# Kernel optimization log

Hardware: AMD Instinct MI355X
Metric: run time of the kernel (lower is better)

## Reference

```python
import jax, jax.numpy as jnp
import numpy as np


def setup_inputs() -> dict:
    key = jax.random.key(0)
    k1, k2, k3 = jax.random.split(key, 3)
    B, H, F, O = 2048, 512, 128, 10
    inputs = jax.random.normal(k1, (B, F), dtype=jnp.float32)
    # centers ~ uniform(-1, 1) as in init_params
    centers = jax.random.uniform(k2, (H, F), dtype=jnp.float32, minval=-1.0, maxval=1.0)
    sigma = jnp.ones((1,), dtype=jnp.float32)
    W = jax.random.normal(k3, (O, H), dtype=jnp.float32) * (1.0 / np.sqrt(H))
    b = jnp.zeros((O,), dtype=jnp.float32)
    return {"inputs": inputs, "centers": centers, "sigma": sigma, "W": W, "b": b}


def reference(inputs, centers, sigma, W, b):
    # pairwise squared distances: [B, H, F] diff -> sum over F -> [B, H]
    diff = inputs[:, None, :] - centers[None, :, :]
    distances = jnp.sum(diff * diff, axis=-1)  # [B, H]
    rbf = jnp.exp(-distances / (2.0 * sigma[0] ** 2))  # [B, H]
    # linear: y = rbf @ W.T + b
    return rbf @ W.T + b
```

## Files before the change

### kernel.cpp

```cpp
#include <hip/hip_runtime.h>


constexpr int Fdim = 128;
constexpr int Hdim = 512;
constexpr int Odim = 10;
constexpr int BM   = 8;
constexpr int KC   = 32;
constexpr int NCH  = Fdim / KC;
constexpr int LDC  = 513;
constexpr int LDXT = 12;
constexpr int LDR  = 516;

__global__ __launch_bounds__(512, 1) void rbf_all(
    const float* __restrict__ x,
    const float* __restrict__ c,
    const float* __restrict__ sigmap,
    const float* __restrict__ W,
    const float* __restrict__ bias,
    float* __restrict__ out)
{
    __shared__ float cT[KC][LDC];
    __shared__ float xT[Fdim][LDXT];
    __shared__ float W_s[Odim][Hdim];
    __shared__ float rbf_s[BM][LDR];
    __shared__ float xn_s[BM];
    __shared__ float cn_s[Hdim];

    const int tid  = threadIdx.x;
    const int lane = tid & 63;
    const int wave = tid >> 6;
    const int wr   = wave >> 2;
    const int wh   = wave & 3;
    const int row0 = blockIdx.x * BM;

    const float4* x4 = reinterpret_cast<const float4*>(x);
    const float4* c4 = reinterpret_cast<const float4*>(c);

#pragma unroll
    for (int k = 0; k < (Odim * Hdim) / 512; ++k) {
        int idx = tid + 512 * k;
        W_s[idx >> 9][idx & 511] = W[idx];
    }

    if (tid < 256) {
        int r  = tid >> 5;
        int fq = tid & 31;
        float4 v = x4[(size_t)(row0 + r) * (Fdim / 4) + fq];
        xT[4 * fq + 0][r] = v.x;
        xT[4 * fq + 1][r] = v.y;
        xT[4 * fq + 2][r] = v.z;
        xT[4 * fq + 3][r] = v.w;
        float s = v.x * v.x + v.y * v.y + v.z * v.z + v.w * v.w;
#pragma unroll
        for (int sft = 1; sft < 32; sft <<= 1) s += __shfl_xor(s, sft, 64);
        if (fq == 0) xn_s[r] = s;
    }

    const int f4 = tid & 7;
    const int hh = tid >> 3;

    float4 pre[8];
    float cn_part[8];
#pragma unroll
    for (int p = 0; p < 8; ++p) cn_part[p] = 0.0f;

#pragma unroll
    for (int p = 0; p < 8; ++p)
        pre[p] = c4[(size_t)(hh + 64 * p) * (Fdim / 4) + f4];
#pragma unroll
    for (int p = 0; p < 8; ++p) {
        float4 v = pre[p];
        int h = hh + 64 * p;
        cT[4 * f4 + 0][h] = v.x;
        cT[4 * f4 + 1][h] = v.y;
        cT[4 * f4 + 2][h] = v.z;
        cT[4 * f4 + 3][h] = v.w;
        cn_part[p] += v.x * v.x + v.y * v.y + v.z * v.z + v.w * v.w;
    }
    __syncthreads();

    float acc[4][2];
#pragma unroll
    for (int i = 0; i < 4; ++i) { acc[i][0] = 0.0f; acc[i][1] = 0.0f; }

    for (int k = 0; k < NCH; ++k) {
        if (k + 1 < NCH) {
#pragma unroll
            for (int p = 0; p < 8; ++p)
                pre[p] = c4[(size_t)(hh + 64 * p) * (Fdim / 4) + (k + 1) * (KC / 4) + f4];
        }

#pragma unroll 8
        for (int f = 0; f < KC; ++f) {
            float4 xv = *reinterpret_cast<const float4*>(&xT[k * KC + f][4 * wr]);
            float2 cv = *reinterpret_cast<const float2*>(&cT[f][wh * 128 + 2 * lane]);
            acc[0][0] = fmaf(xv.x, cv.x, acc[0][0]);
            acc[0][1] = fmaf(xv.x, cv.y, acc[0][1]);
            acc[1][0] = fmaf(xv.y, cv.x, acc[1][0]);
            acc[1][1] = fmaf(xv.y, cv.y, acc[1][1]);
            acc[2][0] = fmaf(xv.z, cv.x, acc[2][0]);
            acc[2][1] = fmaf(xv.z, cv.y, acc[2][1]);
            acc[3][0] = fmaf(xv.w, cv.x, acc[3][0]);
            acc[3][1] = fmaf(xv.w, cv.y, acc[3][1]);
        }

        if (k + 1 < NCH) {
            __syncthreads();
#pragma unroll
            for (int p = 0; p < 8; ++p) {
                float4 v = pre[p];
                int h = hh + 64 * p;
                cT[4 * f4 + 0][h] = v.x;
                cT[4 * f4 + 1][h] = v.y;
                cT[4 * f4 + 2][h] = v.z;
                cT[4 * f4 + 3][h] = v.w;
                cn_part[p] += v.x * v.x + v.y * v.y + v.z * v.z + v.w * v.w;
            }
            __syncthreads();
        }
    }

#pragma unroll
    for (int p = 0; p < 8; ++p) {
        float s = cn_part[p];
        s += __shfl_xor(s, 1, 64);
        s += __shfl_xor(s, 2, 64);
        s += __shfl_xor(s, 4, 64);
        cn_part[p] = s;
    }
    if (f4 == 0) {
#pragma unroll
        for (int p = 0; p < 8; ++p) cn_s[hh + 64 * p] = cn_part[p];
    }
    __syncthreads();

    const float sg    = sigmap[0];
    const float scale = -1.0f / (2.0f * sg * sg);
    {
        float2 cn = *reinterpret_cast<const float2*>(&cn_s[wh * 128 + 2 * lane]);
#pragma unroll
        for (int i = 0; i < 4; ++i) {
            float xn = xn_s[4 * wr + i];
            float2 rv;
            rv.x = __expf((xn + cn.x - 2.0f * acc[i][0]) * scale);
            rv.y = __expf((xn + cn.y - 2.0f * acc[i][1]) * scale);
            *reinterpret_cast<float2*>(&rbf_s[4 * wr + i][wh * 128 + 2 * lane]) = rv;
        }
    }
    __syncthreads();

    {
        const int row = wave;
        float po[Odim];
#pragma unroll
        for (int o = 0; o < Odim; ++o) po[o] = 0.0f;

#pragma unroll
        for (int k = 0; k < 8; ++k) {
            int h = lane + 64 * k;
            float r = rbf_s[row][h];
#pragma unroll
            for (int o = 0; o < Odim; ++o)
                po[o] = fmaf(r, W_s[o][h], po[o]);
        }
#pragma unroll
        for (int s = 1; s < 64; s <<= 1) {
#pragma unroll
            for (int o = 0; o < Odim; ++o)
                po[o] += __shfl_xor(po[o], s, 64);
        }
        if (lane == 0) {
#pragma unroll
            for (int o = 0; o < Odim; ++o)
                out[(size_t)(row0 + row) * Odim + o] = po[o] + bias[o];
        }
    }
}

extern "C" void kernel_launch(void* const* d_in, const int* in_sizes, int n_in,
                              void* d_out, int out_size, void* d_ws, size_t ws_size,
                              hipStream_t stream) {
    const float* x  = (const float*)d_in[0];
    const float* c  = (const float*)d_in[1];
    const float* sg = (const float*)d_in[2];
    const float* W  = (const float*)d_in[3];
    const float* b  = (const float*)d_in[4];
    float* out      = (float*)d_out;

    const int B = in_sizes[0] / Fdim;

    rbf_all<<<B / BM, 512, 0, stream>>>(x, c, sg, W, b, out);
}
```

Baseline: 17.65 us.

## Give each thread one center and read x rows straight from global memory

The transposed shared-memory copies of x and centers are replaced. Each thread now owns one hidden unit and keeps a row-major, XOR-swizzled float4 tile of its center in shared memory. The x rows are loaded directly from global memory as wave-uniform float4s, with the next group prefetched in registers, and each thread accumulates 8 row dot products. This removes the x transpose and the scattered cT stores. In exchange it issues many redundant global loads of x per thread, relying on cache and broadcast, and uses more registers.

```diff
diff --git a/kernel.cpp b/kernel.cpp
--- a/kernel.cpp
+++ b/kernel.cpp
@@ -7,8 +7,6 @@
 constexpr int BM   = 8;
 constexpr int KC   = 32;
 constexpr int NCH  = Fdim / KC;
-constexpr int LDC  = 513;
-constexpr int LDXT = 12;
 constexpr int LDR  = 516;
 
 __global__ __launch_bounds__(512, 1) void rbf_all(
@@ -19,8 +17,7 @@
     const float* __restrict__ bias,
     float* __restrict__ out)
 {
-    __shared__ float cT[KC][LDC];
-    __shared__ float xT[Fdim][LDXT];
+    __shared__ float c_s[Hdim * KC];
     __shared__ float W_s[Odim][Hdim];
     __shared__ float rbf_s[BM][LDR];
     __shared__ float xn_s[BM];
@@ -29,8 +26,6 @@
     const int tid  = threadIdx.x;
     const int lane = tid & 63;
     const int wave = tid >> 6;
-    const int wr   = wave >> 2;
-    const int wh   = wave & 3;
     const int row0 = blockIdx.x * BM;
 
     const float4* x4 = reinterpret_cast<const float4*>(x);
@@ -46,18 +41,14 @@
         int r  = tid >> 5;
         int fq = tid & 31;
         float4 v = x4[(size_t)(row0 + r) * (Fdim / 4) + fq];
-        xT[4 * fq + 0][r] = v.x;
-        xT[4 * fq + 1][r] = v.y;
-        xT[4 * fq + 2][r] = v.z;
-        xT[4 * fq + 3][r] = v.w;
         float s = v.x * v.x + v.y * v.y + v.z * v.z + v.w * v.w;
 #pragma unroll
         for (int sft = 1; sft < 32; sft <<= 1) s += __shfl_xor(s, sft, 64);
         if (fq == 0) xn_s[r] = s;
     }
 
-    const int f4 = tid & 7;
-    const int hh = tid >> 3;
+    const int sfq = tid & 7;
+    const int sh  = tid >> 3;
 
     float4 pre[8];
     float cn_part[8];
@@ -66,42 +57,63 @@
 
 #pragma unroll
     for (int p = 0; p < 8; ++p)
-        pre[p] = c4[(size_t)(hh + 64 * p) * (Fdim / 4) + f4];
+        pre[p] = c4[(size_t)(sh + 64 * p) * (Fdim / 4) + sfq];
 #pragma unroll
     for (int p = 0; p < 8; ++p) {
         float4 v = pre[p];
-        int h = hh + 64 * p;
-        cT[4 * f4 + 0][h] = v.x;
-        cT[4 * f4 + 1][h] = v.y;
-        cT[4 * f4 + 2][h] = v.z;
-        cT[4 * f4 + 3][h] = v.w;
+        int h = sh + 64 * p;
+        *reinterpret_cast<float4*>(&c_s[h * KC + ((sfq ^ (h & 7)) << 2)]) = v;
         cn_part[p] += v.x * v.x + v.y * v.y + v.z * v.z + v.w * v.w;
     }
     __syncthreads();
 
-    float acc[4][2];
+    float acc[8];
 #pragma unroll
-    for (int i = 0; i < 4; ++i) { acc[i][0] = 0.0f; acc[i][1] = 0.0f; }
+    for (int r = 0; r < 8; ++r) acc[r] = 0.0f;
+
+    const int hown = tid;
+    const int hswz = hown & 7;
+
+    float4 xc[8];
+#pragma unroll
+    for (int r = 0; r < 8; ++r)
+        xc[r] = x4[(size_t)(row0 + r) * (Fdim / 4) + 0];
 
     for (int k = 0; k < NCH; ++k) {
         if (k + 1 < NCH) {
 #pragma unroll
             for (int p = 0; p < 8; ++p)
-                pre[p] = c4[(size_t)(hh + 64 * p) * (Fdim / 4) + (k + 1) * (KC / 4) + f4];
+                pre[p] = c4[(size_t)(sh + 64 * p) * (Fdim / 4) + (k + 1) * (KC / 4) + sfq];
         }
 
-#pragma unroll 8
-        for (int f = 0; f < KC; ++f) {
-            float4 xv = *reinterpret_cast<const float4*>(&xT[k * KC + f][4 * wr]);
-            float2 cv = *reinterpret_cast<const float2*>(&cT[f][wh * 128 + 2 * lane]);
-            acc[0][0] = fmaf(xv.x, cv.x, acc[0][0]);
-            acc[0][1] = fmaf(xv.x, cv.y, acc[0][1]);
-            acc[1][0] = fmaf(xv.y, cv.x, acc[1][0]);
-            acc[1][1] = fmaf(xv.y, cv.y, acc[1][1]);
-            acc[2][0] = fmaf(xv.z, cv.x, acc[2][0]);
-            acc[2][1] = fmaf(xv.z, cv.y, acc[2][1]);
-            acc[3][0] = fmaf(xv.w, cv.x, acc[3][0]);
-            acc[3][1] = fmaf(xv.w, cv.y, acc[3][1]);
+#pragma unroll
+        for (int fg = 0; fg < KC / 4; ++fg) {
+            float4 xnx[8];
+            {
+                int nk = k, nfg = fg + 1;
+                if (nfg == KC / 4) { nfg = 0; nk = k + 1; }
+                if (nk < NCH) {
+#pragma unroll
+                    for (int r = 0; r < 8; ++r)
+                        xnx[r] = x4[(size_t)(row0 + r) * (Fdim / 4) + nk * (KC / 4) + nfg];
+                } else {
+#pragma unroll
+                    for (int r = 0; r < 8; ++r) xnx[r] = xc[r];
+                }
+            }
+
+            float4 cv = *reinterpret_cast<const float4*>(
+                &c_s[hown * KC + ((fg ^ hswz) << 2)]);
+
+#pragma unroll
+            for (int r = 0; r < 8; ++r) {
+                acc[r] = fmaf(xc[r].x, cv.x, acc[r]);
+                acc[r] = fmaf(xc[r].y, cv.y, acc[r]);
+                acc[r] = fmaf(xc[r].z, cv.z, acc[r]);
+                acc[r] = fmaf(xc[r].w, cv.w, acc[r]);
+            }
+#pragma unroll
+            for (int r = 0; r < 8; ++r) xc[r] = xnx[r];
         }
 
         if (k + 1 < NCH) {
@@ -109,11 +121,8 @@
 #pragma unroll
             for (int p = 0; p < 8; ++p) {
                 float4 v = pre[p];
-                int h = hh + 64 * p;
-                cT[4 * f4 + 0][h] = v.x;
-                cT[4 * f4 + 1][h] = v.y;
-                cT[4 * f4 + 2][h] = v.z;
-                cT[4 * f4 + 3][h] = v.w;
+                int h = sh + 64 * p;
+                *reinterpret_cast<float4*>(&c_s[h * KC + ((sfq ^ (h & 7)) << 2)]) = v;
                 cn_part[p] += v.x * v.x + v.y * v.y + v.z * v.z + v.w * v.w;
             }
             __syncthreads();
@@ -128,23 +137,20 @@
         s += __shfl_xor(s, 4, 64);
         cn_part[p] = s;
     }
-    if (f4 == 0) {
+    if (sfq == 0) {
 #pragma unroll
-        for (int p = 0; p < 8; ++p) cn_s[hh + 64 * p] = cn_part[p];
+        for (int p = 0; p < 8; ++p) cn_s[sh + 64 * p] = cn_part[p];
     }
     __syncthreads();
 
     const float sg    = sigmap[0];
     const float scale = -1.0f / (2.0f * sg * sg);
     {
-        float2 cn = *reinterpret_cast<const float2*>(&cn_s[wh * 128 + 2 * lane]);
+        float cn = cn_s[hown];
 #pragma unroll
-        for (int i = 0; i < 4; ++i) {
-            float xn = xn_s[4 * wr + i];
-            float2 rv;
-            rv.x = __expf((xn + cn.x - 2.0f * acc[i][0]) * scale);
-            rv.y = __expf((xn + cn.y - 2.0f * acc[i][1]) * scale);
-            *reinterpret_cast<float2*>(&rbf_s[4 * wr + i][wh * 128 + 2 * lane]) = rv;
+        for (int r = 0; r < 8; ++r) {
+            float d = xn_s[r] + cn - 2.0f * acc[r];
+            rbf_s[r][hown] = __expf(d * scale);
         }
     }
     __syncthreads();
```

Result: slower. 26.05 us (+47.6%).

## Double-buffer center chunks in shared memory and register-load W for output

Applied to the files above, without the earlier changes.

Replaces the single padded transposed center tile with a double-buffered shared tile of half the chunk size, so writing the next chunk overlaps with compute and needs only one barrier per chunk. Center loads become vectorized float4 transposes, and the norm partials are reduced through a small shared array instead of shuffles. W is loaded directly into registers rather than staged in shared memory. The output reduction uses a shorter shuffle tree followed by a shared-memory cross-group sum. The aim is fewer barriers, less LDS traffic and better overlap, at the cost of more registers and an extra final barrier.

```diff
diff --git a/kernel.cpp b/kernel.cpp
--- a/kernel.cpp
+++ b/kernel.cpp
@@ -5,11 +5,9 @@
 constexpr int Hdim = 512;
 constexpr int Odim = 10;
 constexpr int BM   = 8;
-constexpr int KC   = 32;
+constexpr int KC   = 16;
 constexpr int NCH  = Fdim / KC;
-constexpr int LDC  = 513;
 constexpr int LDXT = 12;
-constexpr int LDR  = 516;
 
 __global__ __launch_bounds__(512, 1) void rbf_all(
     const float* __restrict__ x,
@@ -19,12 +17,12 @@
     const float* __restrict__ bias,
     float* __restrict__ out)
 {
-    __shared__ float cT[KC][LDC];
+    __shared__ float c_s[2][KC][Hdim];
     __shared__ float xT[Fdim][LDXT];
-    __shared__ float W_s[Odim][Hdim];
-    __shared__ float rbf_s[BM][LDR];
+    __shared__ float rbf_s[BM][Hdim];
+    __shared__ float cn_tmp[4][Hdim];
+    __shared__ float po_s[BM][8][Odim];
     __shared__ float xn_s[BM];
-    __shared__ float cn_s[Hdim];
 
     const int tid  = threadIdx.x;
     const int lane = tid & 63;
@@ -35,12 +33,6 @@
 
     const float4* x4 = reinterpret_cast<const float4*>(x);
     const float4* c4 = reinterpret_cast<const float4*>(c);
-
-#pragma unroll
-    for (int k = 0; k < (Odim * Hdim) / 512; ++k) {
-        int idx = tid + 512 * k;
-        W_s[idx >> 9][idx & 511] = W[idx];
-    }
 
     if (tid < 256) {
         int r  = tid >> 5;
@@ -56,27 +48,42 @@
         if (fq == 0) xn_s[r] = s;
     }
 
-    const int f4 = tid & 7;
-    const int hh = tid >> 3;
-
-    float4 pre[8];
-    float cn_part[8];
-#pragma unroll
-    for (int p = 0; p < 8; ++p) cn_part[p] = 0.0f;
-
-#pragma unroll
-    for (int p = 0; p < 8; ++p)
-        pre[p] = c4[(size_t)(hh + 64 * p) * (Fdim / 4) + f4];
-#pragma unroll
-    for (int p = 0; p < 8; ++p) {
-        float4 v = pre[p];
-        int h = hh + 64 * p;
-        cT[4 * f4 + 0][h] = v.x;
-        cT[4 * f4 + 1][h] = v.y;
-        cT[4 * f4 + 2][h] = v.z;
-        cT[4 * f4 + 3][h] = v.w;
-        cn_part[p] += v.x * v.x + v.y * v.y + v.z * v.z + v.w * v.w;
-    }
+    const int fq = tid >> 7;
+    const int hq = tid & 127;
+
+    float4 pre[4];
+    float cnp[4] = {0.0f, 0.0f, 0.0f, 0.0f};
+
+#define CLOAD(k)                                                              \
+    {                                                                         \
+        _Pragma("unroll")                                                     \
+        for (int i = 0; i < 4; ++i)                                           \
+            pre[i] = c4[(size_t)(4 * hq + i) * (Fdim / 4) + (k) * 4 + fq];    \
+    }
+
+#define CWRITE(k)                                                             \
+    {                                                                         \
+        float a0[4] = {pre[0].x, pre[0].y, pre[0].z, pre[0].w};               \
+        float a1[4] = {pre[1].x, pre[1].y, pre[1].z, pre[1].w};               \
+        float a2[4] = {pre[2].x, pre[2].y, pre[2].z, pre[2].w};               \
+        float a3[4] = {pre[3].x, pre[3].y, pre[3].z, pre[3].w};               \
+        _Pragma("unroll")                                                     \
+        for (int j = 0; j < 4; ++j) {                                         \
+            float4 w4;                                                        \
+            w4.x = a0[j]; w4.y = a1[j]; w4.z = a2[j]; w4.w = a3[j];           \
+            *reinterpret_cast<float4*>(&c_s[(k) & 1][4 * fq + j][4 * hq]) = w4; \
+        }                                                                     \
+        cnp[0] += pre[0].x * pre[0].x + pre[0].y * pre[0].y +                 \
+                  pre[0].z * pre[0].z + pre[0].w * pre[0].w;                  \
+        cnp[1] += pre[1].x * pre[1].x + pre[1].y * pre[1].y +                 \
+                  pre[1].z * pre[1].z + pre[1].w * pre[1].w;                  \
+        cnp[2] += pre[2].x * pre[2].x + pre[2].y * pre[2].y +                 \
+                  pre[2].z * pre[2].z + pre[2].w * pre[2].w;                  \
+        cnp[3] += pre[3].x * pre[3].x + pre[3].y * pre[3].y +                 \
+                  pre[3].z * pre[3].z + pre[3].w * pre[3].w;                  \
+    }
+
+    CLOAD(0); CWRITE(0); CLOAD(1);
     __syncthreads();
 
     float acc[4][2];
@@ -84,16 +91,14 @@
     for (int i = 0; i < 4; ++i) { acc[i][0] = 0.0f; acc[i][1] = 0.0f; }
 
     for (int k = 0; k < NCH; ++k) {
-        if (k + 1 < NCH) {
-#pragma unroll
-            for (int p = 0; p < 8; ++p)
-                pre[p] = c4[(size_t)(hh + 64 * p) * (Fdim / 4) + (k + 1) * (KC / 4) + f4];
-        }
-
-#pragma unroll 8
+        if (k + 1 < NCH) CWRITE(k + 1);
+        if (k + 2 < NCH) CLOAD(k + 2);
+
+#pragma unroll
         for (int f = 0; f < KC; ++f) {
             float4 xv = *reinterpret_cast<const float4*>(&xT[k * KC + f][4 * wr]);
-            float2 cv = *reinterpret_cast<const float2*>(&cT[f][wh * 128 + 2 * lane]);
+            float2 cv = *reinterpret_cast<const float2*>(
+                &c_s[k & 1][f][wh * 128 + 2 * lane]);
             acc[0][0] = fmaf(xv.x, cv.x, acc[0][0]);
             acc[0][1] = fmaf(xv.x, cv.y, acc[0][1]);
             acc[1][0] = fmaf(xv.y, cv.x, acc[1][0]);
@@ -103,41 +108,34 @@
             acc[3][0] = fmaf(xv.w, cv.x, acc[3][0]);
             acc[3][1] = fmaf(xv.w, cv.y, acc[3][1]);
         }
-
-        if (k + 1 < NCH) {
-            __syncthreads();
-#pragma unroll
-            for (int p = 0; p < 8; ++p) {
-                float4 v = pre[p];
-                int h = hh + 64 * p;
-                cT[4 * f4 + 0][h] = v.x;
-                cT[4 * f4 + 1][h] = v.y;
-                cT[4 * f4 + 2][h] = v.z;
-                cT[4 * f4 + 3][h] = v.w;
-                cn_part[p] += v.x * v.x + v.y * v.y + v.z * v.z + v.w * v.w;
-            }
-            __syncthreads();
-        }
-    }
-
-#pragma unroll
-    for (int p = 0; p < 8; ++p) {
-        float s = cn_part[p];
-        s += __shfl_xor(s, 1, 64);
-        s += __shfl_xor(s, 2, 64);
-        s += __shfl_xor(s, 4, 64);
-        cn_part[p] = s;
-    }
-    if (f4 == 0) {
-#pragma unroll
-        for (int p = 0; p < 8; ++p) cn_s[hh + 64 * p] = cn_part[p];
-    }
+        __syncthreads();
+    }
+#undef CLOAD
+#undef CWRITE
+
+    float2 W2[Odim][4];
+#pragma unroll
+    for (int o = 0; o < Odim; ++o)
+#pragma unroll
+        for (int k = 0; k < 4; ++k)
+            W2[o][k] = *reinterpret_cast<const float2*>(
+                &W[o * Hdim + 2 * lane + 128 * k]);
+
+#pragma unroll
+    for (int i = 0; i < 4; ++i) cn_tmp[fq][4 * hq + i] = cnp[i];
     __syncthreads();
 
     const float sg    = sigmap[0];
     const float scale = -1.0f / (2.0f * sg * sg);
     {
-        float2 cn = *reinterpret_cast<const float2*>(&cn_s[wh * 128 + 2 * lane]);
+        float2 cn;
+        cn.x = 0.0f; cn.y = 0.0f;
+#pragma unroll
+        for (int q = 0; q < 4; ++q) {
+            float2 t = *reinterpret_cast<const float2*>(
+                &cn_tmp[q][wh * 128 + 2 * lane]);
+            cn.x += t.x; cn.y += t.y;
+        }
 #pragma unroll
         for (int i = 0; i < 4; ++i) {
             float xn = xn_s[4 * wr + i];
@@ -156,24 +154,36 @@
         for (int o = 0; o < Odim; ++o) po[o] = 0.0f;
 
 #pragma unroll
-        for (int k = 0; k < 8; ++k) {
-            int h = lane + 64 * k;
-            float r = rbf_s[row][h];
-#pragma unroll
-            for (int o = 0; o < Odim; ++o)
-                po[o] = fmaf(r, W_s[o][h], po[o]);
-        }
-#pragma unroll
-        for (int s = 1; s < 64; s <<= 1) {
+        for (int k = 0; k < 4; ++k) {
+            float2 rv = *reinterpret_cast<const float2*>(
+                &rbf_s[row][2 * lane + 128 * k]);
+#pragma unroll
+            for (int o = 0; o < Odim; ++o) {
+                po[o] = fmaf(rv.x, W2[o][k].x, po[o]);
+                po[o] = fmaf(rv.y, W2[o][k].y, po[o]);
+            }
+        }
+#pragma unroll
+        for (int s = 1; s < 8; s <<= 1) {
 #pragma unroll
             for (int o = 0; o < Odim; ++o)
                 po[o] += __shfl_xor(po[o], s, 64);
         }
-        if (lane == 0) {
+        if ((lane & 7) == 0) {
 #pragma unroll
             for (int o = 0; o < Odim; ++o)
-                out[(size_t)(row0 + row) * Odim + o] = po[o] + bias[o];
-        }
+                po_s[row][lane >> 3][o] = po[o];
+        }
+    }
+    __syncthreads();
+
+    if (tid < BM * Odim) {
+        int w = tid / Odim;
+        int o = tid - w * Odim;
+        float v = bias[o];
+#pragma unroll
+        for (int g = 0; g < 8; ++g) v += po_s[w][g][o];
+        out[(size_t)(row0 + w) * Odim + o] = v;
     }
 }
 
```

New measurement: 20.50 us. 16.1% more time.
